# Optimization experiments

Measured on AMD Instinct MI355X. Metric: run time of the kernel, lower is better.

Reference implementation:

```python
import jax, jax.numpy as jnp
import numpy as np

N_SUB = 16
IN, OUT, WIDTH, DEPTH = 1, 1, 128, 4  # DEPTH-1 hidden->hidden layers
EPS = 1e-8
FT = 0.3  # fixed_transition
N_PTS = 65536


def setup_inputs() -> dict:
    key = jax.random.key(0)
    ks = jax.random.split(key, 8)
    x = jax.random.uniform(ks[0], (N_PTS, IN), dtype=jnp.float32)

    # overlapping subdomains tiling [0,1]
    i = jnp.arange(N_SUB, dtype=jnp.float32)
    xmins = (i / N_SUB - 0.05)[:, None]          # (S, 1)
    xmaxs = ((i + 1) / N_SUB + 0.05)[:, None]    # (S, 1)
    t = jnp.log((1 - EPS) / EPS)
    w = jnp.full_like(xmins, FT)
    mu_min = xmins + w / 2
    sd_min = w / (2 * t)
    mu_max = xmaxs - w / 2
    sd_max = w / (2 * t)
    centres = (xmins + xmaxs) / 2
    scales = (xmaxs - xmins) / 2

    s_in = 1.0 / np.sqrt(IN)
    s_h = 1.0 / np.sqrt(WIDTH)
    W0 = jax.random.normal(ks[1], (N_SUB, WIDTH, IN), jnp.float32) * s_in
    b0 = jnp.zeros((N_SUB, WIDTH), jnp.float32)
    Wh = jax.random.normal(ks[2], (N_SUB, DEPTH - 1, WIDTH, WIDTH), jnp.float32) * s_h
    bh = jnp.zeros((N_SUB, DEPTH - 1, WIDTH), jnp.float32)
    Wout = jax.random.normal(ks[3], (N_SUB, OUT, WIDTH), jnp.float32) * s_h
    bout = jnp.zeros((N_SUB, OUT), jnp.float32)

    return dict(x=x, W0=W0, b0=b0, Wh=Wh, bh=bh, Wout=Wout, bout=bout,
                centres=centres, scales=scales,
                mu_min=mu_min, sd_min=sd_min, mu_max=mu_max, sd_max=sd_max)


def reference(x, W0, b0, Wh, bh, Wout, bout, centres, scales,
              mu_min, sd_min, mu_max, sd_max):
    # window weights: partition-of-unity sigmoids on first coordinate  (S, N)
    x0 = x[None, :, 0]                                   # (1, N)
    w_lo = jax.nn.sigmoid((x0 - mu_min[:, 0:1]) / sd_min[:, 0:1])
    w_hi = jax.nn.sigmoid((mu_max[:, 0:1] - x0) / sd_max[:, 0:1])
    wm = w_lo * w_hi                                     # (S, N)

    # per-subnet normalised inputs  (S, N, IN)
    xi = (x[None, :, :] - centres[:, None, :]) / jnp.maximum(scales, EPS)[:, None, :]

    # batched small MLP over subnets (tanh hidden, linear head)
    h = jnp.tanh(jnp.einsum('swi,sni->snw', W0, xi) + b0[:, None, :])
    for l in range(DEPTH - 1):
        h = jnp.tanh(jnp.einsum('svw,snw->snv', Wh[:, l], h) + bh[:, l, None, :])
    raw = (jnp.einsum('sow,snw->sno', Wout, h) + bout[:, None, :])[..., 0]  # (S, N)

    # windowed sum over subnets -> (N, 1)
    return jnp.sum(wm * raw, axis=0)[:, None]
```

## Files before the change

kernel.cpp:

```cpp
#include <hip/hip_runtime.h>
#include <hip/hip_bf16.h>
#include <math.h>

#define NPTS   65536
#define NS     16
#define WID    128
#define NHID   3
#define CAP    24576
#define ROWB   272
#define CZ     -25.33f
#define CSTR   32

#define OFF_IDX 2048
#define OFF_WF  (OFF_IDX + NS * CAP * 4)
#define OFF_WO  (OFF_WF + NS * NHID * WID * WID * 2)

typedef _Float16 f16x8 __attribute__((ext_vector_type(8)));
typedef _Float16 f16x4 __attribute__((ext_vector_type(4)));
typedef float    f32x4 __attribute__((ext_vector_type(4)));

__device__ __forceinline__ float tanh5(float x) {
    float e = __builtin_amdgcn_exp2f(x * 2.8853900817779268f);
    float r = __builtin_amdgcn_rcpf(e + 1.f);
    return fmaf(-2.f, r, 1.f);
}
__device__ __forceinline__ float sigmf(float z) {
    float e = __builtin_amdgcn_exp2f(-z * 1.4426950408889634f);
    return __builtin_amdgcn_rcpf(1.f + e);
}

__global__ void init_kernel(int* __restrict__ counts,
                            const float* __restrict__ Wh, _Float16* __restrict__ WF,
                            const float* __restrict__ Wout, _Float16* __restrict__ WoutF) {
    int b = blockIdx.x, t = threadIdx.x;
    if (b == 0 && t < NS) counts[t * CSTR] = 0;
    if (b < 384) {
        int g = b * 256 + t;
        int sl = g >> 11, r = g & 2047;
        int vt = r >> 8, kk = (r >> 6) & 3, lane = r & 63;
        int v = vt * 16 + (lane & 15);
        int w0 = kk * 32 + (lane >> 4) * 8;
        const float* src = Wh + (sl << 14) + v * WID + w0;
        float4 a = *(const float4*)src;
        float4 c = *(const float4*)(src + 4);
        f16x8 o;
        o[0] = (_Float16)a.x; o[1] = (_Float16)a.y; o[2] = (_Float16)a.z; o[3] = (_Float16)a.w;
        o[4] = (_Float16)c.x; o[5] = (_Float16)c.y; o[6] = (_Float16)c.z; o[7] = (_Float16)c.w;
        ((f16x8*)WF)[g] = o;
    } else {
        int g = (b - 384) * 256 + t;
        int s = g >> 8, kk = (g >> 6) & 3, lane = g & 63;
        f16x8 o = (f16x8)(_Float16)0.f;
        if ((lane & 15) == 0) {
            int w0 = kk * 32 + (lane >> 4) * 8;
            const float* src = Wout + s * WID + w0;
            float4 a = *(const float4*)src;
            float4 c = *(const float4*)(src + 4);
            o[0] = (_Float16)a.x; o[1] = (_Float16)a.y; o[2] = (_Float16)a.z; o[3] = (_Float16)a.w;
            o[4] = (_Float16)c.x; o[5] = (_Float16)c.y; o[6] = (_Float16)c.z; o[7] = (_Float16)c.w;
        }
        ((f16x8*)WoutF)[g] = o;
    }
}

__global__ void bucket_kernel(const float* __restrict__ x,
                              const float* __restrict__ mu_min, const float* __restrict__ sd_min,
                              const float* __restrict__ mu_max, const float* __restrict__ sd_max,
                              int* counts, int* __restrict__ idx,
                              float* __restrict__ out) {
    __shared__ int wcnt[NS][4];
    __shared__ int wbase[NS][4];
    __shared__ int bbase[NS];
    int t = threadIdx.x, lane = t & 63, wid = t >> 6;
    int n = blockIdx.x * 256 + t;
    float xv = x[n];
    out[n] = 0.f;
    unsigned long long ltmask = (1ULL << lane) - 1ULL;
    unsigned mbits = 0;
    #pragma unroll
    for (int s = 0; s < NS; ++s) {
        float z1 = __fdividef(xv - mu_min[s], sd_min[s]);
        float z2 = __fdividef(mu_max[s] - xv, sd_max[s]);
        bool m = (z1 > CZ) && (z2 > CZ);
        mbits |= (unsigned)m << s;
        unsigned long long mk = __ballot(m);
        if (lane == 0) wcnt[s][wid] = __popcll(mk);
    }
    __syncthreads();
    if (t < NS) {
        int c0 = wcnt[t][0], c1 = wcnt[t][1], c2 = wcnt[t][2], c3 = wcnt[t][3];
        wbase[t][0] = 0; wbase[t][1] = c0; wbase[t][2] = c0 + c1; wbase[t][3] = c0 + c1 + c2;
        bbase[t] = atomicAdd(&counts[t * CSTR], c0 + c1 + c2 + c3);
    }
    __syncthreads();
    #pragma unroll
    for (int s = 0; s < NS; ++s) {
        bool m = (mbits >> s) & 1;
        unsigned long long mk = __ballot(m);
        if (m) {
            int pos = __popcll(mk & ltmask);
            int g = bbase[s] + wbase[s][wid] + pos;
            if (g < CAP) idx[s * CAP + g] = n;
        }
    }
}

__global__ __launch_bounds__(512, 8) void mlp_kernel(
        const float* __restrict__ x,
        const float* __restrict__ W0,   const float* __restrict__ b0,
        const _Float16* __restrict__ WF, const float* __restrict__ bh,
        const _Float16* __restrict__ WoutF, const float* __restrict__ bout,
        const float* __restrict__ centres, const float* __restrict__ scales,
        const float* __restrict__ mu_min,  const float* __restrict__ sd_min,
        const float* __restrict__ mu_max,  const float* __restrict__ sd_max,
        const int* __restrict__ counts, const int* __restrict__ idx,
        float* __restrict__ out) {
    __shared__ __align__(16) char hbuf[2][64 * ROWB];
    __shared__ float xi_s[64], wm_s[64];
    __shared__ int   nn_s[64];

    int s = blockIdx.x;
    int cnt = counts[s * CSTR]; if (cnt > CAP) cnt = CAP;
    int base = blockIdx.y * 64;
    if (base >= cnt) return;
    int t = threadIdx.x;

    if (t < 64) {
        int p = base + t;
        float xi = 0.f, wmv = 0.f; int n = 0;
        if (p < cnt) {
            n = idx[s * CAP + p];
            float xv = x[n];
            float wl = sigmf(__fdividef(xv - mu_min[s], sd_min[s]));
            float wh = sigmf(__fdividef(mu_max[s] - xv, sd_max[s]));
            wmv = wl * wh;
            xi = __fdividef(xv - centres[s], fmaxf(scales[s], 1e-8f));
        }
        xi_s[t] = xi; wm_s[t] = wmv; nn_s[t] = n;
    }
    __syncthreads();

    int lane = t & 63, w = t >> 6;
    int lr = lane & 15, lg = lane >> 4;
    int vq = w & 3, ph = w >> 2;

    {
        int p = lane, v0 = w * 16;
        float xi = xi_s[p];
        const float4* W04 = (const float4*)(W0 + s * WID + v0);
        const float4* b04 = (const float4*)(b0 + s * WID + v0);
        char* row = hbuf[0] + p * ROWB + v0 * 2;
        #pragma unroll
        for (int k = 0; k < 2; ++k) {
            float4 wa = W04[k * 2],     ba = b04[k * 2];
            float4 wb = W04[k * 2 + 1], bb = b04[k * 2 + 1];
            f16x8 hv;
            hv[0] = (_Float16)tanh5(fmaf(wa.x, xi, ba.x));
            hv[1] = (_Float16)tanh5(fmaf(wa.y, xi, ba.y));
            hv[2] = (_Float16)tanh5(fmaf(wa.z, xi, ba.z));
            hv[3] = (_Float16)tanh5(fmaf(wa.w, xi, ba.w));
            hv[4] = (_Float16)tanh5(fmaf(wb.x, xi, bb.x));
            hv[5] = (_Float16)tanh5(fmaf(wb.y, xi, bb.y));
            hv[6] = (_Float16)tanh5(fmaf(wb.z, xi, bb.z));
            hv[7] = (_Float16)tanh5(fmaf(wb.w, xi, bb.w));
            *(f16x8*)(row + k * 16) = hv;
        }
    }

    int cur = 0;
    for (int l = 0; l < NHID; ++l) {
        __syncthreads();
        const f16x8* WFp = (const f16x8*)WF + (size_t)(s * NHID + l) * 2048;
        const float* bhp = bh + (s * NHID + l) * WID;
        f32x4 acc[2][2];
        #pragma unroll
        for (int i = 0; i < 2; ++i) {
            int v0 = vq * 32 + i * 16 + lg * 4;
            f32x4 binit = *(const f32x4*)(bhp + v0);
            acc[i][0] = binit; acc[i][1] = binit;
        }
        const char* hb = hbuf[cur];
        #pragma unroll
        for (int kk = 0; kk < 4; ++kk) {
            f16x8 a0 = WFp[((vq * 2 + 0) * 4 + kk) * 64 + lane];
            f16x8 a1 = WFp[((vq * 2 + 1) * 4 + kk) * 64 + lane];
            #pragma unroll
            for (int j = 0; j < 2; ++j) {
                f16x8 b = *(const f16x8*)(hb + (ph * 32 + j * 16 + lr) * ROWB + kk * 64 + lg * 16);
                acc[0][j] = __builtin_amdgcn_mfma_f32_16x16x32_f16(a0, b, acc[0][j], 0, 0, 0);
                acc[1][j] = __builtin_amdgcn_mfma_f32_16x16x32_f16(a1, b, acc[1][j], 0, 0, 0);
            }
        }
        char* ho = hbuf[cur ^ 1];
        #pragma unroll
        for (int i = 0; i < 2; ++i) {
            int vo = vq * 32 + i * 16 + lg * 4;
            #pragma unroll
            for (int j = 0; j < 2; ++j) {
                f32x4 a = acc[i][j];
                f16x4 qv;
                qv[0] = (_Float16)tanh5(a[0]);
                qv[1] = (_Float16)tanh5(a[1]);
                qv[2] = (_Float16)tanh5(a[2]);
                qv[3] = (_Float16)tanh5(a[3]);
                *(f16x4*)(ho + (ph * 32 + j * 16 + lr) * ROWB + vo * 2) = qv;
            }
        }
        cur ^= 1;
    }
    __syncthreads();

    if (w < 4) {
        const char* hf = hbuf[cur];
        float bo = bout[s];
        f32x4 oacc = (f32x4){bo, bo, bo, bo};
        const f16x8* WOp = (const f16x8*)WoutF + s * 256;
        #pragma unroll
        for (int kk = 0; kk < 4; ++kk) {
            f16x8 a = WOp[kk * 64 + lane];
            f16x8 b = *(const f16x8*)(hf + (w * 16 + lr) * ROWB + kk * 64 + lg * 16);
            oacc = __builtin_amdgcn_mfma_f32_16x16x32_f16(a, b, oacc, 0, 0, 0);
        }
        if (lg == 0) {
            int p = w * 16 + lr;
            if (base + p < cnt) atomicAdd(&out[nn_s[p]], wm_s[p] * oacc[0]);
        }
    }
}

extern "C" void kernel_launch(void* const* d_in, const int* in_sizes, int n_in,
                              void* d_out, int out_size, void* d_ws, size_t ws_size,
                              hipStream_t stream) {
    const float* x       = (const float*)d_in[0];
    const float* W0      = (const float*)d_in[1];
    const float* b0      = (const float*)d_in[2];
    const float* Wh      = (const float*)d_in[3];
    const float* bh      = (const float*)d_in[4];
    const float* Wout    = (const float*)d_in[5];
    const float* bout    = (const float*)d_in[6];
    const float* centres = (const float*)d_in[7];
    const float* scales  = (const float*)d_in[8];
    const float* mu_min  = (const float*)d_in[9];
    const float* sd_min  = (const float*)d_in[10];
    const float* mu_max  = (const float*)d_in[11];
    const float* sd_max  = (const float*)d_in[12];
    float* out = (float*)d_out;
    char* ws = (char*)d_ws;
    int*      counts = (int*)ws;
    int*      idx    = (int*)(ws + OFF_IDX);
    _Float16* WF     = (_Float16*)(ws + OFF_WF);
    _Float16* WoutF  = (_Float16*)(ws + OFF_WO);

    init_kernel<<<dim3(400), dim3(256), 0, stream>>>(counts, Wh, WF, Wout, WoutF);
    bucket_kernel<<<dim3(NPTS / 256), dim3(256), 0, stream>>>(x, mu_min, sd_min, mu_max, sd_max,
                                                              counts, idx, out);
    dim3 grid(NS, CAP / 64);
    mlp_kernel<<<grid, dim3(512), 0, stream>>>(x, W0, b0, WF, bh, WoutF, bout,
                                               centres, scales, mu_min, sd_min, mu_max, sd_max,
                                               counts, idx, out);
}
```

Baseline: 146.9 us.

## Make each wave own 16 points end-to-end, removing block-wide syncs

Result: slower. 173.8 us (+18.4%).

```diff
diff --git a/kernel.cpp b/kernel.cpp
--- a/kernel.cpp
+++ b/kernel.cpp
@@ -7,7 +7,6 @@
 #define WID    128
 #define NHID   3
 #define CAP    24576
-#define ROWB   272
 #define CZ     -25.33f
 #define CSTR   32
 
@@ -105,7 +104,7 @@
     }
 }
 
-__global__ __launch_bounds__(512, 8) void mlp_kernel(
+__global__ __launch_bounds__(256, 5) void mlp_kernel(
         const float* __restrict__ x,
         const float* __restrict__ W0,   const float* __restrict__ b0,
         const _Float16* __restrict__ WF, const float* __restrict__ bh,
@@ -115,116 +114,85 @@
         const float* __restrict__ mu_max,  const float* __restrict__ sd_max,
         const int* __restrict__ counts, const int* __restrict__ idx,
         float* __restrict__ out) {
-    __shared__ __align__(16) char hbuf[2][64 * ROWB];
-    __shared__ float xi_s[64], wm_s[64];
-    __shared__ int   nn_s[64];
+    __shared__ __align__(16) char scr[4][4096];
 
     int s = blockIdx.x;
     int cnt = counts[s * CSTR]; if (cnt > CAP) cnt = CAP;
-    int base = blockIdx.y * 64;
+    int t = threadIdx.x, lane = t & 63, w = t >> 6;
+    int base = blockIdx.y * 64 + w * 16;
     if (base >= cnt) return;
-    int t = threadIdx.x;
-
-    if (t < 64) {
-        int p = base + t;
-        float xi = 0.f, wmv = 0.f; int n = 0;
-        if (p < cnt) {
-            n = idx[s * CAP + p];
-            float xv = x[n];
-            float wl = sigmf(__fdividef(xv - mu_min[s], sd_min[s]));
-            float wh = sigmf(__fdividef(mu_max[s] - xv, sd_max[s]));
-            wmv = wl * wh;
-            xi = __fdividef(xv - centres[s], fmaxf(scales[s], 1e-8f));
-        }
-        xi_s[t] = xi; wm_s[t] = wmv; nn_s[t] = n;
-    }
-    __syncthreads();
-
-    int lane = t & 63, w = t >> 6;
-    int lr = lane & 15, lg = lane >> 4;
-    int vq = w & 3, ph = w >> 2;
-
-    {
-        int p = lane, v0 = w * 16;
-        float xi = xi_s[p];
-        const float4* W04 = (const float4*)(W0 + s * WID + v0);
-        const float4* b04 = (const float4*)(b0 + s * WID + v0);
-        char* row = hbuf[0] + p * ROWB + v0 * 2;
-        #pragma unroll
-        for (int k = 0; k < 2; ++k) {
-            float4 wa = W04[k * 2],     ba = b04[k * 2];
-            float4 wb = W04[k * 2 + 1], bb = b04[k * 2 + 1];
-            f16x8 hv;
-            hv[0] = (_Float16)tanh5(fmaf(wa.x, xi, ba.x));
-            hv[1] = (_Float16)tanh5(fmaf(wa.y, xi, ba.y));
-            hv[2] = (_Float16)tanh5(fmaf(wa.z, xi, ba.z));
-            hv[3] = (_Float16)tanh5(fmaf(wa.w, xi, ba.w));
-            hv[4] = (_Float16)tanh5(fmaf(wb.x, xi, bb.x));
-            hv[5] = (_Float16)tanh5(fmaf(wb.y, xi, bb.y));
-            hv[6] = (_Float16)tanh5(fmaf(wb.z, xi, bb.z));
-            hv[7] = (_Float16)tanh5(fmaf(wb.w, xi, bb.w));
-            *(f16x8*)(row + k * 16) = hv;
-        }
-    }
-
-    int cur = 0;
+    int g = lane >> 4, p = lane & 15;
+    int swz = (p & 7) << 4;
+    char* S = scr[w];
+
+    int slot = base + p;
+    bool live = slot < cnt;
+    int n = 0; float xi = 0.f, wmv = 0.f;
+    if (live) {
+        n = idx[s * CAP + slot];
+        float xv = x[n];
+        float wl = sigmf(__fdividef(xv - mu_min[s], sd_min[s]));
+        float wh = sigmf(__fdividef(mu_max[s] - xv, sd_max[s]));
+        wmv = wl * wh;
+        xi = __fdividef(xv - centres[s], fmaxf(scales[s], 1e-8f));
+    }
+
+    f16x8 B[4];
+    const float* W0p = W0 + s * WID;
+    const float* b0p = b0 + s * WID;
+    #pragma unroll
+    for (int kk = 0; kk < 4; ++kk) {
+        int v0 = kk * 32 + g * 8;
+        float4 wa = *(const float4*)(W0p + v0), wb = *(const float4*)(W0p + v0 + 4);
+        float4 ba = *(const float4*)(b0p + v0), bb = *(const float4*)(b0p + v0 + 4);
+        f16x8 hv;
+        hv[0] = (_Float16)tanh5(fmaf(wa.x, xi, ba.x));
+        hv[1] = (_Float16)tanh5(fmaf(wa.y, xi, ba.y));
+        hv[2] = (_Float16)tanh5(fmaf(wa.z, xi, ba.z));
+        hv[3] = (_Float16)tanh5(fmaf(wa.w, xi, ba.w));
+        hv[4] = (_Float16)tanh5(fmaf(wb.x, xi, bb.x));
+        hv[5] = (_Float16)tanh5(fmaf(wb.y, xi, bb.y));
+        hv[6] = (_Float16)tanh5(fmaf(wb.z, xi, bb.z));
+        hv[7] = (_Float16)tanh5(fmaf(wb.w, xi, bb.w));
+        B[kk] = hv;
+    }
+
     for (int l = 0; l < NHID; ++l) {
-        __syncthreads();
         const f16x8* WFp = (const f16x8*)WF + (size_t)(s * NHID + l) * 2048;
         const float* bhp = bh + (s * NHID + l) * WID;
-        f32x4 acc[2][2];
-        #pragma unroll
-        for (int i = 0; i < 2; ++i) {
-            int v0 = vq * 32 + i * 16 + lg * 4;
-            f32x4 binit = *(const f32x4*)(bhp + v0);
-            acc[i][0] = binit; acc[i][1] = binit;
-        }
-        const char* hb = hbuf[cur];
-        #pragma unroll
-        for (int kk = 0; kk < 4; ++kk) {
-            f16x8 a0 = WFp[((vq * 2 + 0) * 4 + kk) * 64 + lane];
-            f16x8 a1 = WFp[((vq * 2 + 1) * 4 + kk) * 64 + lane];
+        f32x4 acc[8];
+        #pragma unroll
+        for (int vt = 0; vt < 8; ++vt) {
+            f32x4 a = *(const f32x4*)(bhp + vt * 16 + g * 4);
             #pragma unroll
-            for (int j = 0; j < 2; ++j) {
-                f16x8 b = *(const f16x8*)(hb + (ph * 32 + j * 16 + lr) * ROWB + kk * 64 + lg * 16);
-                acc[0][j] = __builtin_amdgcn_mfma_f32_16x16x32_f16(a0, b, acc[0][j], 0, 0, 0);
-                acc[1][j] = __builtin_amdgcn_mfma_f32_16x16x32_f16(a1, b, acc[1][j], 0, 0, 0);
+            for (int kk = 0; kk < 4; ++kk) {
+                f16x8 af = WFp[(vt * 4 + kk) * 64 + lane];
+                a = __builtin_amdgcn_mfma_f32_16x16x32_f16(af, B[kk], a, 0, 0, 0);
             }
-        }
-        char* ho = hbuf[cur ^ 1];
-        #pragma unroll
-        for (int i = 0; i < 2; ++i) {
-            int vo = vq * 32 + i * 16 + lg * 4;
-            #pragma unroll
-            for (int j = 0; j < 2; ++j) {
-                f32x4 a = acc[i][j];
-                f16x4 qv;
-                qv[0] = (_Float16)tanh5(a[0]);
-                qv[1] = (_Float16)tanh5(a[1]);
-                qv[2] = (_Float16)tanh5(a[2]);
-                qv[3] = (_Float16)tanh5(a[3]);
-                *(f16x4*)(ho + (ph * 32 + j * 16 + lr) * ROWB + vo * 2) = qv;
-            }
-        }
-        cur ^= 1;
-    }
-    __syncthreads();
-
-    if (w < 4) {
-        const char* hf = hbuf[cur];
+            acc[vt] = a;
+        }
+        #pragma unroll
+        for (int vt = 0; vt < 8; ++vt) {
+            f16x4 q;
+            q[0] = (_Float16)tanh5(acc[vt][0]);
+            q[1] = (_Float16)tanh5(acc[vt][1]);
+            q[2] = (_Float16)tanh5(acc[vt][2]);
+            q[3] = (_Float16)tanh5(acc[vt][3]);
+            *(f16x4*)(S + p * 256 + ((((g * 4 + vt * 16) * 2)) ^ swz)) = q;
+        }
+        #pragma unroll
+        for (int kk = 0; kk < 4; ++kk)
+            B[kk] = *(const f16x8*)(S + p * 256 + ((((kk * 32 + g * 8) * 2)) ^ swz));
+    }
+
+    {
         float bo = bout[s];
         f32x4 oacc = (f32x4){bo, bo, bo, bo};
         const f16x8* WOp = (const f16x8*)WoutF + s * 256;
         #pragma unroll
-        for (int kk = 0; kk < 4; ++kk) {
-            f16x8 a = WOp[kk * 64 + lane];
-            f16x8 b = *(const f16x8*)(hf + (w * 16 + lr) * ROWB + kk * 64 + lg * 16);
-            oacc = __builtin_amdgcn_mfma_f32_16x16x32_f16(a, b, oacc, 0, 0, 0);
-        }
-        if (lg == 0) {
-            int p = w * 16 + lr;
-            if (base + p < cnt) atomicAdd(&out[nn_s[p]], wm_s[p] * oacc[0]);
-        }
+        for (int kk = 0; kk < 4; ++kk)
+            oacc = __builtin_amdgcn_mfma_f32_16x16x32_f16(WOp[kk * 64 + lane], B[kk], oacc, 0, 0, 0);
+        if (g == 0 && live) atomicAdd(&out[n], wmv * oacc[0]);
     }
 }
 
@@ -255,7 +223,7 @@
     bucket_kernel<<<dim3(NPTS / 256), dim3(256), 0, stream>>>(x, mu_min, sd_min, mu_max, sd_max,
                                                               counts, idx, out);
     dim3 grid(NS, CAP / 64);
-    mlp_kernel<<<grid, dim3(512), 0, stream>>>(x, W0, b0, WF, bh, WoutF, bout,
+    mlp_kernel<<<grid, dim3(256), 0, stream>>>(x, W0, b0, WF, bh, WoutF, bout,
                                                centres, scales, mu_min, sd_min, mu_max, sd_max,
                                                counts, idx, out);
 }
```
